# Performance work log

Measured on AMD Instinct MI355X. Metric: run time of the kernel, lower is better.

## Reference

```python
import jax, jax.numpy as jnp
import numpy as np

B, S, D = 2, 2048, 2048
H, KV, HD = 16, 8, 128
N_REP = H // KV


def _rotate_half(x):
    x1, x2 = x[..., : x.shape[-1] // 2], x[..., x.shape[-1] // 2 :]
    return jnp.concatenate((-x2, x1), axis=-1)


def setup_inputs() -> dict:
    key = jax.random.key(0)
    ks = jax.random.split(key, 5)
    x = jax.random.normal(ks[0], (B, S, D), dtype=jnp.float32)
    # rotary tables (llama-style): inv_freq over half dims, duplicated
    inv_freq = 1.0 / (10000.0 ** (jnp.arange(0, HD, 2, dtype=jnp.float32) / HD))
    t = jnp.arange(S, dtype=jnp.float32)
    freqs = jnp.outer(t, inv_freq)                      # [S, HD/2]
    emb = jnp.concatenate((freqs, freqs), axis=-1)      # [S, HD]
    cos, sin = jnp.cos(emb), jnp.sin(emb)
    sc = 0.02
    Wq = jax.random.normal(ks[1], (D, H * HD), dtype=jnp.float32) * sc
    Wk = jax.random.normal(ks[2], (D, KV * HD), dtype=jnp.float32) * sc
    Wv = jax.random.normal(ks[3], (D, KV * HD), dtype=jnp.float32) * sc
    Wo = jax.random.normal(ks[4], (H * HD, D), dtype=jnp.float32) * sc
    return {"x": x, "cos": cos, "sin": sin, "Wq": Wq, "Wk": Wk, "Wv": Wv, "Wo": Wo}


def reference(x, cos, sin, Wq, Wk, Wv, Wo):
    b, s, _ = x.shape
    q = (x @ Wq).reshape(b, s, H, HD)
    k = (x @ Wk).reshape(b, s, KV, HD)
    v = (x @ Wv).reshape(b, s, KV, HD)
    # RoPE (broadcast over batch and heads; unsqueeze_dim=2 layout [b,s,h,d])
    c = cos[None, :, None, :]
    sn = sin[None, :, None, :]
    q = q * c + _rotate_half(q) * sn
    k = k * c + _rotate_half(k) * sn
    # GQA expansion (repeat_kv == interleaved repeat along head dim)
    k = jnp.repeat(k, N_REP, axis=2)
    v = jnp.repeat(v, N_REP, axis=2)
    scale = HD ** -0.5
    # causal attention (single-rank ring attention == one causal flash block)
    scores = jnp.einsum("bqhd,bkhd->bhqk", q, k) * scale
    mask = jnp.tril(jnp.ones((s, s), dtype=bool))
    scores = jnp.where(mask[None, None], scores, -jnp.inf)
    probs = jax.nn.softmax(scores, axis=-1)
    attn = jnp.einsum("bhqk,bkhd->bqhd", probs, v).reshape(b, s, H * HD)
    return attn @ Wo
```

## Files before the change

kernel.cpp:

```cpp
#include <hip/hip_runtime.h>


typedef __bf16 bf16;
typedef __bf16 bf16x4 __attribute__((ext_vector_type(4)));
typedef __bf16 bf16x8 __attribute__((ext_vector_type(8)));
typedef float floatx4 __attribute__((ext_vector_type(4)));

#define AS1(p) ((const __attribute__((address_space(1))) void*)(p))
#define AS3(p) ((__attribute__((address_space(3))) void*)(p))

__device__ __forceinline__ void load16(const void* g, void* l) {
  __builtin_amdgcn_global_load_lds(AS1(g), AS3(l), 16, 0, 0);
}

__device__ __forceinline__ void phase_barrier() {
  asm volatile("" ::: "memory");
  __builtin_amdgcn_sched_barrier(0);
  __builtin_amdgcn_s_barrier();
  __builtin_amdgcn_sched_barrier(0);
  asm volatile("" ::: "memory");
}

__global__ __launch_bounds__(256) void cvt_kernel(const float* __restrict__ in,
                                                  bf16* __restrict__ out, int n4) {
  int i = blockIdx.x * blockDim.x + threadIdx.x;
  if (i >= n4) return;
  float4 v = ((const float4*)in)[i];
  bf16x4 o = {(bf16)v.x, (bf16)v.y, (bf16)v.z, (bf16)v.w};
  ((bf16x4*)out)[i] = o;
}

__global__ __launch_bounds__(256) void wtrans_kernel(
    const float* __restrict__ Wq, const float* __restrict__ Wk,
    const float* __restrict__ Wv, const float* __restrict__ Wo,
    bf16* __restrict__ WqkvT, bf16* __restrict__ WoT) {
  __shared__ float tile[32][33];
  const int wid = blockIdx.z;
  const float* src = wid == 0 ? Wq : wid == 1 ? Wk : wid == 2 ? Wv : Wo;
  bf16* dst = wid == 0 ? WqkvT
            : wid == 1 ? WqkvT + 2048ull * 2048
            : wid == 2 ? WqkvT + 3072ull * 2048
                       : WoT;
  const int ncols = (wid == 1 || wid == 2) ? 1024 : 2048;
  const int c0 = blockIdx.x * 32, r0 = blockIdx.y * 32;
  if (c0 >= ncols) return;
  const int tx = threadIdx.x & 31, ty = threadIdx.x >> 5;
#pragma unroll
  for (int i = 0; i < 4; i++) {
    int ri = ty + i * 8;
    tile[ri][tx] = src[(long)(r0 + ri) * ncols + c0 + tx];
  }
  __syncthreads();
#pragma unroll
  for (int i = 0; i < 4; i++) {
    int ci = ty + i * 8;
    dst[(long)(c0 + ci) * 2048 + r0 + tx] = (bf16)tile[tx][ci];
  }
}

__global__ __launch_bounds__(256) void transpose_bf16(
    const bf16* __restrict__ in, bf16* __restrict__ out,
    int ldi, int ldo, long ibs, long obs) {
  __shared__ bf16 tile[32][33];
  const long ib = ibs * blockIdx.z, ob = obs * blockIdx.z;
  const int c0 = blockIdx.x * 32, r0 = blockIdx.y * 32;
  const int tx = threadIdx.x & 31, ty = threadIdx.x >> 5;
#pragma unroll
  for (int i = 0; i < 4; i++) {
    int ri = ty + i * 8;
    tile[ri][tx] = in[ib + (long)(r0 + ri) * ldi + c0 + tx];
  }
  __syncthreads();
#pragma unroll
  for (int i = 0; i < 4; i++) {
    int ci = ty + i * 8;
    out[ob + (long)(c0 + ci) * ldo + r0 + tx] = tile[tx][ci];
  }
}

template <typename CT>
__global__ __launch_bounds__(512, 2) void gemm256(
    const bf16* __restrict__ A, const bf16* __restrict__ Bt, CT* __restrict__ C,
    int M, int N, int K) {
  __shared__ __align__(1024) char smem[131072];
  const int tid = threadIdx.x;
  const int wave = tid >> 6, lane = tid & 63;
  const int quad = lane >> 4, l16 = lane & 15;
  const int wm = wave >> 2, wn = wave & 3;
  const int m0 = blockIdx.y * 256, n0 = blockIdx.x * 256;

  const int srow = (wave >> 1) * 16 + (lane >> 2);
  const int skcol = (wave & 1) * 32 + (((lane & 3) * 8) ^ ((lane & 32) ? 16 : 0));
  const int sblk = wave * 1024;

  const int qoff = (quad * 16) ^ ((l16 & 8) << 2);
  const int aoff = wm * 16384 + l16 * 64 + qoff;
  const int boff = 32768 + (wn >> 1) * 16384 + (wn & 1) * 8192 + l16 * 64 + qoff;

  auto stageA = [&](int kt, int h, int buf) {
    const bf16* g = A + (size_t)(m0 + h * 128 + srow) * K + kt * 64 + skcol;
    char* d = smem + buf * 65536 + h * 16384 + sblk;
    load16(g, d);
    load16(g + (size_t)64 * K, d + 8192);
  };
  auto stageB = [&](int kt, int h, int buf) {
    const bf16* g = Bt + (size_t)(n0 + h * 128 + srow) * K + kt * 64 + skcol;
    char* d = smem + buf * 65536 + 32768 + h * 16384 + sblk;
    load16(g, d);
    load16(g + (size_t)64 * K, d + 8192);
  };
  auto rdA = [&](int buf, int fr, int ks) {
    return *(const bf16x8*)(smem + buf * 65536 + aoff + (fr * 2 + ks) * 1024);
  };
  auto rdB = [&](int buf, int fc, int ks) {
    return *(const bf16x8*)(smem + buf * 65536 + boff + (fc * 2 + ks) * 1024);
  };

  floatx4 acc[8][4] = {};

  const int nkt = K >> 6;
  const int niter = nkt >> 1;

  stageB(0, 0, 0); stageB(0, 1, 0);
  stageA(0, 0, 0); stageA(0, 1, 0);
  stageB(1, 0, 1); stageB(1, 1, 1);
  asm volatile("s_waitcnt vmcnt(4)" ::: "memory");
  phase_barrier();

  for (int it = 0; it < niter; ++it) {
    const int T = 2 * it;
    const bool morek = (it < niter - 1);
#pragma unroll
    for (int c = 0; c < 2; ++c) {
      const int buf = c;
      const int tA = T + 1 + c;
      const int tB = T + 2 + c;
      const bool stA = (c == 0) || morek;

      bf16x8 a[4][2], b01[2][2], b23[2][2];

#pragma unroll
      for (int fr = 0; fr < 4; ++fr)
#pragma unroll
        for (int ks = 0; ks < 2; ++ks) a[fr][ks] = rdA(buf, fr, ks);
#pragma unroll
      for (int fc = 0; fc < 2; ++fc)
#pragma unroll
        for (int ks = 0; ks < 2; ++ks) b01[fc][ks] = rdB(buf, fc, ks);
      if (stA) stageA(tA, 0, buf ^ 1);
      phase_barrier();
      __builtin_amdgcn_s_setprio(1);
#pragma unroll
      for (int ks = 0; ks < 2; ++ks)
#pragma unroll
        for (int fr = 0; fr < 4; ++fr)
#pragma unroll
          for (int fc = 0; fc < 2; ++fc)
            acc[fr][fc] = __builtin_amdgcn_mfma_f32_16x16x32_bf16(
                a[fr][ks], b01[fc][ks], acc[fr][fc], 0, 0, 0);
      __builtin_amdgcn_s_setprio(0);
      phase_barrier();

#pragma unroll
      for (int fc = 0; fc < 2; ++fc)
#pragma unroll
        for (int ks = 0; ks < 2; ++ks) b23[fc][ks] = rdB(buf, 2 + fc, ks);
      if (stA) stageA(tA, 1, buf ^ 1);
      phase_barrier();
      __builtin_amdgcn_s_setprio(1);
#pragma unroll
      for (int ks = 0; ks < 2; ++ks)
#pragma unroll
        for (int fr = 0; fr < 4; ++fr)
#pragma unroll
          for (int fc = 0; fc < 2; ++fc)
            acc[fr][2 + fc] = __builtin_amdgcn_mfma_f32_16x16x32_bf16(
                a[fr][ks], b23[fc][ks], acc[fr][2 + fc], 0, 0, 0);
      __builtin_amdgcn_s_setprio(0);
      phase_barrier();

#pragma unroll
      for (int fr = 0; fr < 4; ++fr)
#pragma unroll
        for (int ks = 0; ks < 2; ++ks) a[fr][ks] = rdA(buf, 4 + fr, ks);
      if (morek) stageB(tB, 0, buf);
      phase_barrier();
      __builtin_amdgcn_s_setprio(1);
#pragma unroll
      for (int ks = 0; ks < 2; ++ks)
#pragma unroll
        for (int fr = 0; fr < 4; ++fr)
#pragma unroll
          for (int fc = 0; fc < 2; ++fc)
            acc[4 + fr][2 + fc] = __builtin_amdgcn_mfma_f32_16x16x32_bf16(
                a[fr][ks], b23[fc][ks], acc[4 + fr][2 + fc], 0, 0, 0);
      __builtin_amdgcn_s_setprio(0);
      phase_barrier();

      if (morek) stageB(tB, 1, buf);
      if (morek)
        asm volatile("s_waitcnt vmcnt(4)" ::: "memory");
      else
        asm volatile("s_waitcnt vmcnt(0)" ::: "memory");
      phase_barrier();
      __builtin_amdgcn_s_setprio(1);
#pragma unroll
      for (int ks = 0; ks < 2; ++ks)
#pragma unroll
        for (int fr = 0; fr < 4; ++fr)
#pragma unroll
          for (int fc = 0; fc < 2; ++fc)
            acc[4 + fr][fc] = __builtin_amdgcn_mfma_f32_16x16x32_bf16(
                a[fr][ks], b01[fc][ks], acc[4 + fr][fc], 0, 0, 0);
      __builtin_amdgcn_s_setprio(0);
      phase_barrier();
    }
  }

#pragma unroll
  for (int fr = 0; fr < 8; ++fr)
#pragma unroll
    for (int fc = 0; fc < 4; ++fc)
#pragma unroll
      for (int r = 0; r < 4; ++r) {
        int row = m0 + wm * 128 + fr * 16 + quad * 4 + r;
        int col = n0 + wn * 64 + fc * 16 + l16;
        C[(size_t)row * N + col] = (CT)acc[fr][fc][r];
      }
}

__global__ void rope_kernel(bf16* __restrict__ QKV, const float* __restrict__ cosb,
                            const float* __restrict__ sinb) {
  int idx = blockIdx.x * blockDim.x + threadIdx.x;
  if (idx >= 6291456) return;
  int nh, nhs, offc;
  if (idx < 4194304) { nh = 16; nhs = 4; offc = 0; }
  else { idx -= 4194304; nh = 8; nhs = 3; offc = 2048; }
  int d = idx & 63;
  int rest = idx >> 6;
  int hh = rest & (nh - 1);
  int bs = rest >> nhs;
  int s = bs & 2047;
  size_t base = (size_t)bs * 4096 + offc + hh * 128;
  float c0 = cosb[s * 128 + d];
  float c1 = cosb[s * 128 + d + 64];
  float s0 = sinb[s * 128 + d];
  float s1 = sinb[s * 128 + d + 64];
  float x0 = (float)QKV[base + d];
  float x1 = (float)QKV[base + d + 64];
  QKV[base + d] = (bf16)(x0 * c0 - x1 * s0);
  QKV[base + d + 64] = (bf16)(x1 * c1 + x0 * s1);
}


template <bool MASK>
__device__ __forceinline__ void attn_step32(
    const bf16* Kc, const bf16* Vc, bf16* Pw, const bf16x8 (&aq)[4],
    const bf16x8& ones, floatx4 (&oacc)[8], floatx4& lacc,
    int k0, int q0w, int l16, int quad) {
  floatx4 sacc[4] = {};
  __builtin_amdgcn_s_setprio(1);
#pragma unroll
  for (int ks = 0; ks < 4; ks++)
#pragma unroll
    for (int j = 0; j < 4; j++) {
      int row = j * 16 + l16;
      bf16x8 bk = *(const bf16x8*)(Kc + row * 128 + (((ks * 4 + quad) ^ (row & 15)) * 8));
      sacc[j] = __builtin_amdgcn_mfma_f32_16x16x32_bf16(aq[ks], bk, sacc[j], 0, 0, 0);
    }
  __builtin_amdgcn_s_setprio(0);
  const float C = 0.12752188659023044f;
#pragma unroll
  for (int r = 0; r < 4; r++) {
    int row = quad * 4 + r;
#pragma unroll
    for (int j = 0; j < 4; j++) {
      float p = exp2f(sacc[j][r] * C);
      if (MASK) {
        int key = k0 + j * 16 + l16;
        if (key > q0w + row) p = 0.f;
      }
      int col = j * 16 + l16;
      Pw[row * 64 + (((col >> 3) ^ (row & 7)) * 8) + (col & 7)] = (bf16)p;
    }
  }
  __builtin_amdgcn_s_setprio(1);
#pragma unroll
  for (int ks = 0; ks < 2; ks++) {
    bf16x8 ap = *(const bf16x8*)(Pw + l16 * 64 + (((ks * 4 + quad) ^ (l16 & 7)) * 8));
    lacc = __builtin_amdgcn_mfma_f32_16x16x32_bf16(ap, ones, lacc, 0, 0, 0);
#pragma unroll
    for (int j = 0; j < 8; j++) {
      int vr = j * 16 + l16;
      bf16x8 bv = *(const bf16x8*)(Vc + vr * 64 + (((ks * 4 + quad) ^ (vr & 7)) * 8));
      oacc[j] = __builtin_amdgcn_mfma_f32_16x16x32_bf16(ap, bv, oacc[j], 0, 0, 0);
    }
  }
  __builtin_amdgcn_s_setprio(0);
}

__global__ __launch_bounds__(256, 2) void flash_kernel(
    const bf16* __restrict__ QKV, const bf16* __restrict__ Vt, bf16* __restrict__ O,
    int* __restrict__ cnt) {
  __shared__ __align__(1024) char smem[73728];
  __shared__ int wsh;
  const int tid = threadIdx.x;
  const int wave = tid >> 6, lane = tid & 63, quad = lane >> 4, l16 = lane & 15;
  const int wbase = tid & ~63;
  const int hloc = wave >> 1, rhalf = wave & 1;
  bf16* Pw = (bf16*)(smem + 65536) + wave * 1024;
  bf16x8 ones;
#pragma unroll
  for (int e = 0; e < 8; e++) ones[e] = (bf16)1.0f;

  for (;;) {
    if (tid == 0) wsh = atomicAdd(cnt, 1);
    __syncthreads();
    const int w = wsh;
    if (w >= 1024) break;
    const int qt = 63 - (w >> 4);
    const int b = (w >> 3) & 1, kvh = w & 7;
    const int h = kvh * 2 + hloc;
    const int q0 = qt * 32;
    const int nkt = (qt >> 1) + 1;

#pragma unroll
    for (int u = 0; u < 4; u++) {
      int g = u * 256 + tid;
      int row = g >> 4, cc = g & 15;
      const bf16* gp = QKV + (size_t)(b * 2048 + q0 + (row & 31)) * 4096 +
                       (kvh * 2 + (row >> 5)) * 128 + ((cc ^ (row & 15)) * 8);
      load16(gp, smem + (u * 256 + wbase) * 16);
    }
    asm volatile("s_waitcnt vmcnt(0)" ::: "memory");
    phase_barrier();
    bf16x8 aq[4];
    {
      int row = hloc * 32 + rhalf * 16 + l16;
#pragma unroll
      for (int ks = 0; ks < 4; ks++)
        aq[ks] = *(const bf16x8*)((const bf16*)smem + row * 128 +
                                  (((ks * 4 + quad) ^ (row & 15)) * 8));
    }
    __syncthreads();

    auto stageKV = [&](int kt, int nb) {
      char* kd = smem + nb * 16384;
      char* vd = smem + 32768 + nb * 16384;
#pragma unroll
      for (int u = 0; u < 4; u++) {
        int g = u * 256 + tid;
        int krow = g >> 4, kcc = g & 15;
        const bf16* kp = QKV + (size_t)(b * 2048 + kt * 64 + krow) * 4096 + 2048 +
                         kvh * 128 + ((kcc ^ (krow & 15)) * 8);
        load16(kp, kd + (u * 256 + wbase) * 16);
        int vrow = g >> 3, vcc = g & 7;
        const bf16* vp = Vt + (size_t)(b * 1024 + kvh * 128 + vrow) * 2048 + kt * 64 +
                         ((vcc ^ (vrow & 7)) * 8);
        load16(vp, vd + (u * 256 + wbase) * 16);
      }
    };

    stageKV(0, 0);

    floatx4 oacc[8] = {};
    floatx4 lacc = {};
    const int q0w = q0 + rhalf * 16;

    for (int kt = 0; kt < nkt; kt++) {
      const int cur = kt & 1;
      if (kt + 1 < nkt) {
        stageKV(kt + 1, cur ^ 1);
        asm volatile("s_waitcnt vmcnt(8)" ::: "memory");
      } else {
        asm volatile("s_waitcnt vmcnt(0)" ::: "memory");
      }
      phase_barrier();
      const bf16* Kc = (const bf16*)(smem + cur * 16384);
      const bf16* Vc = (const bf16*)(smem + 32768 + cur * 16384);
      if (kt == nkt - 1)
        attn_step32<true>(Kc, Vc, Pw, aq, ones, oacc, lacc, kt * 64, q0w, l16, quad);
      else
        attn_step32<false>(Kc, Vc, Pw, aq, ones, oacc, lacc, kt * 64, q0w, l16, quad);
      phase_barrier();
    }

    float rl[4];
#pragma unroll
    for (int r = 0; r < 4; r++) rl[r] = 1.0f / lacc[r];
#pragma unroll
    for (int j = 0; j < 8; j++)
#pragma unroll
      for (int r = 0; r < 4; r++) {
        int s = q0w + quad * 4 + r;
        O[(size_t)(b * 2048 + s) * 2048 + h * 128 + j * 16 + l16] =
            (bf16)(oacc[j][r] * rl[r]);
      }
  }
}

extern "C" void kernel_launch(void* const* d_in, const int* in_sizes, int n_in,
                              void* d_out, int out_size, void* d_ws, size_t ws_size,
                              hipStream_t stream) {
  (void)in_sizes; (void)n_in; (void)out_size; (void)ws_size;
  const float* x    = (const float*)d_in[0];
  const float* cosb = (const float*)d_in[1];
  const float* sinb = (const float*)d_in[2];
  const float* Wq   = (const float*)d_in[3];
  const float* Wk   = (const float*)d_in[4];
  const float* Wv   = (const float*)d_in[5];
  const float* Wo   = (const float*)d_in[6];
  float* out = (float*)d_out;

  char* ws = (char*)d_ws;
  size_t off = 0;
  auto alloc = [&](size_t bytes) { void* p = ws + off; off += bytes; return p; };
  bf16* xb    = (bf16*)alloc(4096ull * 2048 * 2);
  bf16* WqkvT = (bf16*)alloc(4096ull * 2048 * 2);
  bf16* WoT   = (bf16*)alloc(2048ull * 2048 * 2);
  bf16* QKV   = (bf16*)alloc(4096ull * 4096 * 2);
  bf16* Vtb   = (bf16*)alloc(2048ull * 2048 * 2);
  bf16* Ab    = (bf16*)alloc(4096ull * 2048 * 2);
  int*  cnt   = (int*)alloc(256);

  cvt_kernel<<<8192, 256, 0, stream>>>(x, xb, 2097152);
  hipMemsetAsync(cnt, 0, 256, stream);

  wtrans_kernel<<<dim3(64, 64, 4), 256, 0, stream>>>(Wq, Wk, Wv, Wo, WqkvT, WoT);

  gemm256<bf16><<<dim3(16, 16), 512, 0, stream>>>(xb, WqkvT, QKV, 4096, 4096, 2048);

  rope_kernel<<<24576, 256, 0, stream>>>(QKV, cosb, sinb);

  transpose_bf16<<<dim3(32, 64, 2), 256, 0, stream>>>(
      QKV + 3072, Vtb, 4096, 2048, 2048ll * 4096, 1024ll * 2048);

  flash_kernel<<<dim3(512, 1, 1), 256, 0, stream>>>(QKV, Vtb, Ab, cnt);

  gemm256<float><<<dim3(8, 16), 512, 0, stream>>>(Ab, WoT, out, 4096, 2048, 2048);
}
```

Measured before the change: 342.6 us.

## Prefetch KV tiles through registers to cut LDS and raise flash occupancy

Result: slower. 378.4 us (+10.5%).

```diff
diff --git a/kernel.cpp b/kernel.cpp
--- a/kernel.cpp
+++ b/kernel.cpp
@@ -299,16 +299,18 @@
   __builtin_amdgcn_s_setprio(0);
 }
 
-__global__ __launch_bounds__(256, 2) void flash_kernel(
+__global__ __launch_bounds__(256, 3) void flash_kernel(
     const bf16* __restrict__ QKV, const bf16* __restrict__ Vt, bf16* __restrict__ O,
     int* __restrict__ cnt) {
-  __shared__ __align__(1024) char smem[73728];
+  __shared__ __align__(1024) char smem[40960];
   __shared__ int wsh;
   const int tid = threadIdx.x;
   const int wave = tid >> 6, lane = tid & 63, quad = lane >> 4, l16 = lane & 15;
   const int wbase = tid & ~63;
   const int hloc = wave >> 1, rhalf = wave & 1;
-  bf16* Pw = (bf16*)(smem + 65536) + wave * 1024;
+  bf16* Pw = (bf16*)(smem + 32768) + wave * 1024;
+  const bf16* Kc = (const bf16*)smem;
+  const bf16* Vc = (const bf16*)(smem + 16384);
   bf16x8 ones;
 #pragma unroll
   for (int e = 0; e < 8; e++) ones[e] = (bf16)1.0f;
@@ -344,45 +346,60 @@
     }
     __syncthreads();
 
-    auto stageKV = [&](int kt, int nb) {
-      char* kd = smem + nb * 16384;
-      char* vd = smem + 32768 + nb * 16384;
-#pragma unroll
-      for (int u = 0; u < 4; u++) {
-        int g = u * 256 + tid;
-        int krow = g >> 4, kcc = g & 15;
-        const bf16* kp = QKV + (size_t)(b * 2048 + kt * 64 + krow) * 4096 + 2048 +
-                         kvh * 128 + ((kcc ^ (krow & 15)) * 8);
-        load16(kp, kd + (u * 256 + wbase) * 16);
-        int vrow = g >> 3, vcc = g & 7;
-        const bf16* vp = Vt + (size_t)(b * 1024 + kvh * 128 + vrow) * 2048 + kt * 64 +
-                         ((vcc ^ (vrow & 7)) * 8);
-        load16(vp, vd + (u * 256 + wbase) * 16);
-      }
-    };
-
-    stageKV(0, 0);
+#pragma unroll
+    for (int u = 0; u < 4; u++) {
+      int g = u * 256 + tid;
+      int krow = g >> 4, kcc = g & 15;
+      const bf16* kp = QKV + (size_t)(b * 2048 + krow) * 4096 + 2048 +
+                       kvh * 128 + ((kcc ^ (krow & 15)) * 8);
+      load16(kp, smem + (u * 256 + wbase) * 16);
+      int vrow = g >> 3, vcc = g & 7;
+      const bf16* vp = Vt + (size_t)(b * 1024 + kvh * 128 + vrow) * 2048 +
+                       ((vcc ^ (vrow & 7)) * 8);
+      load16(vp, smem + 16384 + (u * 256 + wbase) * 16);
+    }
+    asm volatile("s_waitcnt vmcnt(0)" ::: "memory");
+    phase_barrier();
 
     floatx4 oacc[8] = {};
     floatx4 lacc = {};
     const int q0w = q0 + rhalf * 16;
 
+    floatx4 kr[4], vr[4];
     for (int kt = 0; kt < nkt; kt++) {
-      const int cur = kt & 1;
-      if (kt + 1 < nkt) {
-        stageKV(kt + 1, cur ^ 1);
-        asm volatile("s_waitcnt vmcnt(8)" ::: "memory");
-      } else {
-        asm volatile("s_waitcnt vmcnt(0)" ::: "memory");
+      const bool pf = (kt + 1 < nkt);
+      if (pf) {
+#pragma unroll
+        for (int u = 0; u < 4; u++) {
+          int g = u * 256 + tid;
+          int krow = g >> 4, kcc = g & 15;
+          const bf16* kp = QKV + (size_t)(b * 2048 + (kt + 1) * 64 + krow) * 4096 +
+                           2048 + kvh * 128 + ((kcc ^ (krow & 15)) * 8);
+          asm volatile("global_load_dwordx4 %0, %1, off"
+                       : "=&v"(kr[u]) : "v"(kp) : "memory");
+          int vrow = g >> 3, vcc = g & 7;
+          const bf16* vp = Vt + (size_t)(b * 1024 + kvh * 128 + vrow) * 2048 +
+                           (kt + 1) * 64 + ((vcc ^ (vrow & 7)) * 8);
+          asm volatile("global_load_dwordx4 %0, %1, off"
+                       : "=&v"(vr[u]) : "v"(vp) : "memory");
+        }
       }
-      phase_barrier();
-      const bf16* Kc = (const bf16*)(smem + cur * 16384);
-      const bf16* Vc = (const bf16*)(smem + 32768 + cur * 16384);
       if (kt == nkt - 1)
         attn_step32<true>(Kc, Vc, Pw, aq, ones, oacc, lacc, kt * 64, q0w, l16, quad);
       else
         attn_step32<false>(Kc, Vc, Pw, aq, ones, oacc, lacc, kt * 64, q0w, l16, quad);
       phase_barrier();
+      if (pf) {
+        asm volatile("s_waitcnt vmcnt(0)" ::: "memory");
+        __builtin_amdgcn_sched_barrier(0);
+#pragma unroll
+        for (int u = 0; u < 4; u++) {
+          *(floatx4*)(smem + (u * 256 + tid) * 16) = kr[u];
+          *(floatx4*)(smem + 16384 + (u * 256 + tid) * 16) = vr[u];
+        }
+        asm volatile("s_waitcnt lgkmcnt(0)" ::: "memory");
+        phase_barrier();
+      }
     }
 
     float rl[4];
@@ -435,7 +452,7 @@
   transpose_bf16<<<dim3(32, 64, 2), 256, 0, stream>>>(
       QKV + 3072, Vtb, 4096, 2048, 2048ll * 4096, 1024ll * 2048);
 
-  flash_kernel<<<dim3(512, 1, 1), 256, 0, stream>>>(QKV, Vtb, Ab, cnt);
+  flash_kernel<<<dim3(768, 1, 1), 256, 0, stream>>>(QKV, Vtb, Ab, cnt);
 
   gemm256<float><<<dim3(8, 16), 512, 0, stream>>>(Ab, WoT, out, 4096, 2048, 2048);
 }
```

## Replace persistent atomic flash scheduler with static 64-row q-tile blocks of 8 waves

Applied to the files above, without the earlier changes.

Measured after the change: 342.1 us. About the same (-0.1%).

```diff
diff --git a/kernel.cpp b/kernel.cpp
--- a/kernel.cpp
+++ b/kernel.cpp
@@ -299,104 +299,97 @@
   __builtin_amdgcn_s_setprio(0);
 }
 
-__global__ __launch_bounds__(256, 2) void flash_kernel(
-    const bf16* __restrict__ QKV, const bf16* __restrict__ Vt, bf16* __restrict__ O,
-    int* __restrict__ cnt) {
-  __shared__ __align__(1024) char smem[73728];
-  __shared__ int wsh;
+__global__ __launch_bounds__(512, 4) void flash_kernel(
+    const bf16* __restrict__ QKV, const bf16* __restrict__ Vt, bf16* __restrict__ O) {
+  __shared__ __align__(1024) char smem[81920];
   const int tid = threadIdx.x;
   const int wave = tid >> 6, lane = tid & 63, quad = lane >> 4, l16 = lane & 15;
   const int wbase = tid & ~63;
-  const int hloc = wave >> 1, rhalf = wave & 1;
+  const int hloc = wave & 1, rgroup = wave >> 1;
   bf16* Pw = (bf16*)(smem + 65536) + wave * 1024;
   bf16x8 ones;
 #pragma unroll
   for (int e = 0; e < 8; e++) ones[e] = (bf16)1.0f;
 
-  for (;;) {
-    if (tid == 0) wsh = atomicAdd(cnt, 1);
-    __syncthreads();
-    const int w = wsh;
-    if (w >= 1024) break;
-    const int qt = 63 - (w >> 4);
-    const int b = (w >> 3) & 1, kvh = w & 7;
-    const int h = kvh * 2 + hloc;
-    const int q0 = qt * 32;
-    const int nkt = (qt >> 1) + 1;
-
-#pragma unroll
-    for (int u = 0; u < 4; u++) {
-      int g = u * 256 + tid;
-      int row = g >> 4, cc = g & 15;
-      const bf16* gp = QKV + (size_t)(b * 2048 + q0 + (row & 31)) * 4096 +
-                       (kvh * 2 + (row >> 5)) * 128 + ((cc ^ (row & 15)) * 8);
-      load16(gp, smem + (u * 256 + wbase) * 16);
-    }
-    asm volatile("s_waitcnt vmcnt(0)" ::: "memory");
+  const int w = blockIdx.x;
+  const int side = w & 1, kvh = (w >> 1) & 7, b = (w >> 4) & 1, g = w >> 5;
+  const int qt = side ? 31 - g : g;
+  const int h = kvh * 2 + hloc;
+  const int q0 = qt * 64;
+  const int nkt = qt + 1;
+
+#pragma unroll
+  for (int u = 0; u < 4; u++) {
+    int gg = u * 512 + tid;
+    int row = gg >> 4, cc = gg & 15;
+    const bf16* gp = QKV + (size_t)(b * 2048 + q0 + (row & 63)) * 4096 +
+                     (kvh * 2 + (row >> 6)) * 128 + ((cc ^ (row & 15)) * 8);
+    load16(gp, smem + (u * 512 + wbase) * 16);
+  }
+  asm volatile("s_waitcnt vmcnt(0)" ::: "memory");
+  phase_barrier();
+  bf16x8 aq[4];
+  {
+    int qr = hloc * 64 + rgroup * 16 + l16;
+#pragma unroll
+    for (int ks = 0; ks < 4; ks++)
+      aq[ks] = *(const bf16x8*)((const bf16*)smem + qr * 128 +
+                                (((ks * 4 + quad) ^ (qr & 15)) * 8));
+  }
+  __syncthreads();
+
+  auto stageKV = [&](int kt, int nb) {
+    char* kd = smem + nb * 16384;
+    char* vd = smem + 32768 + nb * 16384;
+#pragma unroll
+    for (int u = 0; u < 2; u++) {
+      int gg = u * 512 + tid;
+      int krow = gg >> 4, kcc = gg & 15;
+      const bf16* kp = QKV + (size_t)(b * 2048 + kt * 64 + krow) * 4096 + 2048 +
+                       kvh * 128 + ((kcc ^ (krow & 15)) * 8);
+      load16(kp, kd + (u * 512 + wbase) * 16);
+      int vrow = gg >> 3, vcc = gg & 7;
+      const bf16* vp = Vt + (size_t)(b * 1024 + kvh * 128 + vrow) * 2048 + kt * 64 +
+                       ((vcc ^ (vrow & 7)) * 8);
+      load16(vp, vd + (u * 512 + wbase) * 16);
+    }
+  };
+
+  stageKV(0, 0);
+
+  floatx4 oacc[8] = {};
+  floatx4 lacc = {};
+  const int q0w = q0 + rgroup * 16;
+
+  for (int kt = 0; kt < nkt; kt++) {
+    const int cur = kt & 1;
+    if (kt + 1 < nkt) {
+      stageKV(kt + 1, cur ^ 1);
+      asm volatile("s_waitcnt vmcnt(4)" ::: "memory");
+    } else {
+      asm volatile("s_waitcnt vmcnt(0)" ::: "memory");
+    }
     phase_barrier();
-    bf16x8 aq[4];
-    {
-      int row = hloc * 32 + rhalf * 16 + l16;
-#pragma unroll
-      for (int ks = 0; ks < 4; ks++)
-        aq[ks] = *(const bf16x8*)((const bf16*)smem + row * 128 +
-                                  (((ks * 4 + quad) ^ (row & 15)) * 8));
-    }
-    __syncthreads();
-
-    auto stageKV = [&](int kt, int nb) {
-      char* kd = smem + nb * 16384;
-      char* vd = smem + 32768 + nb * 16384;
-#pragma unroll
-      for (int u = 0; u < 4; u++) {
-        int g = u * 256 + tid;
-        int krow = g >> 4, kcc = g & 15;
-        const bf16* kp = QKV + (size_t)(b * 2048 + kt * 64 + krow) * 4096 + 2048 +
-                         kvh * 128 + ((kcc ^ (krow & 15)) * 8);
-        load16(kp, kd + (u * 256 + wbase) * 16);
-        int vrow = g >> 3, vcc = g & 7;
-        const bf16* vp = Vt + (size_t)(b * 1024 + kvh * 128 + vrow) * 2048 + kt * 64 +
-                         ((vcc ^ (vrow & 7)) * 8);
-        load16(vp, vd + (u * 256 + wbase) * 16);
-      }
-    };
-
-    stageKV(0, 0);
-
-    floatx4 oacc[8] = {};
-    floatx4 lacc = {};
-    const int q0w = q0 + rhalf * 16;
-
-    for (int kt = 0; kt < nkt; kt++) {
-      const int cur = kt & 1;
-      if (kt + 1 < nkt) {
-        stageKV(kt + 1, cur ^ 1);
-        asm volatile("s_waitcnt vmcnt(8)" ::: "memory");
-      } else {
-        asm volatile("s_waitcnt vmcnt(0)" ::: "memory");
-      }
-      phase_barrier();
-      const bf16* Kc = (const bf16*)(smem + cur * 16384);
-      const bf16* Vc = (const bf16*)(smem + 32768 + cur * 16384);
-      if (kt == nkt - 1)
-        attn_step32<true>(Kc, Vc, Pw, aq, ones, oacc, lacc, kt * 64, q0w, l16, quad);
-      else
-        attn_step32<false>(Kc, Vc, Pw, aq, ones, oacc, lacc, kt * 64, q0w, l16, quad);
-      phase_barrier();
-    }
-
-    float rl[4];
-#pragma unroll
-    for (int r = 0; r < 4; r++) rl[r] = 1.0f / lacc[r];
-#pragma unroll
-    for (int j = 0; j < 8; j++)
-#pragma unroll
-      for (int r = 0; r < 4; r++) {
-        int s = q0w + quad * 4 + r;
-        O[(size_t)(b * 2048 + s) * 2048 + h * 128 + j * 16 + l16] =
-            (bf16)(oacc[j][r] * rl[r]);
-      }
-  }
+    const bf16* Kc = (const bf16*)(smem + cur * 16384);
+    const bf16* Vc = (const bf16*)(smem + 32768 + cur * 16384);
+    if (kt == nkt - 1)
+      attn_step32<true>(Kc, Vc, Pw, aq, ones, oacc, lacc, kt * 64, q0w, l16, quad);
+    else
+      attn_step32<false>(Kc, Vc, Pw, aq, ones, oacc, lacc, kt * 64, q0w, l16, quad);
+    phase_barrier();
+  }
+
+  float rl[4];
+#pragma unroll
+  for (int r = 0; r < 4; r++) rl[r] = 1.0f / lacc[r];
+#pragma unroll
+  for (int j = 0; j < 8; j++)
+#pragma unroll
+    for (int r = 0; r < 4; r++) {
+      int s = q0w + quad * 4 + r;
+      O[(size_t)(b * 2048 + s) * 2048 + h * 128 + j * 16 + l16] =
+          (bf16)(oacc[j][r] * rl[r]);
+    }
 }
 
 extern "C" void kernel_launch(void* const* d_in, const int* in_sizes, int n_in,
@@ -421,10 +414,8 @@
   bf16* QKV   = (bf16*)alloc(4096ull * 4096 * 2);
   bf16* Vtb   = (bf16*)alloc(2048ull * 2048 * 2);
   bf16* Ab    = (bf16*)alloc(4096ull * 2048 * 2);
-  int*  cnt   = (int*)alloc(256);
 
   cvt_kernel<<<8192, 256, 0, stream>>>(x, xb, 2097152);
-  hipMemsetAsync(cnt, 0, 256, stream);
 
   wtrans_kernel<<<dim3(64, 64, 4), 256, 0, stream>>>(Wq, Wk, Wv, Wo, WqkvT, WoT);
 
@@ -435,7 +426,7 @@
   transpose_bf16<<<dim3(32, 64, 2), 256, 0, stream>>>(
       QKV + 3072, Vtb, 4096, 2048, 2048ll * 4096, 1024ll * 2048);
 
-  flash_kernel<<<dim3(512, 1, 1), 256, 0, stream>>>(QKV, Vtb, Ab, cnt);
+  flash_kernel<<<dim3(512, 1, 1), 512, 0, stream>>>(QKV, Vtb, Ab);
 
   gemm256<float><<<dim3(8, 16), 512, 0, stream>>>(Ab, WoT, out, 4096, 2048, 2048);
 }
```
